# Kernel tuning notes

Hardware: AMD Instinct MI355X
Metric: run time of the kernel (lower is better)

## Reference

```python
import jax, jax.numpy as jnp
import numpy as np

NUM_PROJS = 7
BLOCK = 256       # HyperAttention block_size
SAMPLE = 256      # HyperAttention sample_size
NUM_HEADS = 16

def _hamming_perm(n):
    a = np.array([0, 1])
    for _ in range(n - 1):
        a = np.concatenate([a, a[::-1] + a.max() + 1])
    return a

_PERM = jnp.asarray(_hamming_perm(NUM_PROJS))           # [128] gray-code-ish bucket reorder
_ENC = (2 ** jnp.arange(NUM_PROJS)).astype(jnp.int32)   # [7]

def _lsh_hash(mat, proj_dir):
    # mat: [B,H,N,d], proj_dir: [d,7] -> bucket ids [B,H,N]
    bits = jnp.einsum('bhnd,dr->bhnr', mat, proj_dir) > 0
    ids = (bits * _ENC).sum(-1)
    return _PERM[ids]

def _attn_lse(q, k, v, scale, bias=None):
    s = jnp.einsum('...qd,...kd->...qk', q, k) * scale
    if bias is not None:
        s = s + bias
    lse = jax.nn.logsumexp(s, axis=-1, keepdims=True)
    o = jnp.einsum('...qk,...kd->...qd', jnp.exp(s - lse), v)
    return o, lse

def _gather(t, idx):
    # gather rows along axis 2: out[b,h,s] = t[b,h,idx[b,h,s]]
    return jnp.take_along_axis(t, idx[..., None], axis=2)

def setup_inputs():
    key = jax.random.key(0)
    ks = jax.random.split(key, 7)
    B, L, D, INNER = 2, 8192, 1024, 1024
    x = jax.random.normal(ks[0], (B, L, D), jnp.float32)
    W_qkv = jax.random.normal(ks[1], (D, 3 * INNER), jnp.float32) / np.sqrt(D)
    b_qkv = jnp.zeros((3 * INNER,), jnp.float32)
    W_proj = jax.random.normal(ks[2], (INNER, D), jnp.float32) / np.sqrt(INNER)
    b_proj = jnp.zeros((D,), jnp.float32)
    proj_dir = jax.random.normal(ks[3], (INNER // NUM_HEADS, NUM_PROJS), jnp.float32)
    sampled_set = jax.random.randint(ks[4], (B, NUM_HEADS, SAMPLE), 0, L)
    return {"x": x, "W_qkv": W_qkv, "b_qkv": b_qkv, "W_proj": W_proj,
            "b_proj": b_proj, "proj_dir": proj_dir, "sampled_set": sampled_set}

def reference(x, W_qkv, b_qkv, W_proj, b_proj, proj_dir, sampled_set):
    B, L, D = x.shape
    qkv = (x @ W_qkv + b_qkv).reshape(B, L, 3, NUM_HEADS, -1).transpose(2, 0, 3, 1, 4)
    q, k, v = qkv[0], qkv[1], qkv[2]                      # [B,H,L,dh]
    dh = q.shape[-1]
    scale = dh ** -0.5
    # 1. sortLSH: stable sort q and k rows by angular-LSH bucket id
    q_idx = jnp.argsort(_lsh_hash(q, proj_dir), axis=2, stable=True)
    k_idx = jnp.argsort(_lsh_hash(k, proj_dir), axis=2, stable=True)
    q_idx_inv = jnp.argsort(q_idx, axis=2, stable=True)   # to restore row order
    qs = _gather(q, q_idx)
    ksort = _gather(k, k_idx)
    vsort = _gather(v, k_idx)
    # block-diagonal exact attention over the sorted order (L % BLOCK == 0 here)
    nb = L // BLOCK
    ab, lb = _attn_lse(qs.reshape(B, NUM_HEADS, nb, BLOCK, dh),
                       ksort.reshape(B, NUM_HEADS, nb, BLOCK, dh),
                       vsort.reshape(B, NUM_HEADS, nb, BLOCK, dh), scale)
    attn_block = ab.reshape(B, NUM_HEADS, L, dh)
    lse_block = lb.reshape(B, NUM_HEADS, L, 1)
    # 2. residual uniformly-sampled attention, masking entries already covered by blocks
    k_sub = _gather(ksort, sampled_set)                   # [B,H,SAMPLE,dh]
    v_sub = _gather(vsort, sampled_set)
    blk_q = jnp.arange(L)[None, None, :, None] // BLOCK   # query block id (query_block_size==BLOCK)
    mask = blk_q == (sampled_set // BLOCK)[:, :, None, :]  # [B,H,L,SAMPLE]
    bias = jnp.where(mask, jnp.finfo(x.dtype).min, 0.0).astype(x.dtype)
    attn_res, lse_res = _attn_lse(qs, k_sub, v_sub, scale, bias)
    lse_res = lse_res + jnp.log(jnp.float32(L) / SAMPLE)  # importance weight n_key/sample_size
    # combine the two attentions via their log-sum-exps
    c = 1.0 / (1.0 + jnp.exp(lse_res - lse_block))
    attn = c * attn_block + (1.0 - c) * attn_res
    out = _gather(attn, q_idx_inv)                        # un-sort rows back to input order
    out = out.transpose(0, 2, 1, 3).reshape(B, L, -1)     # [B,L,inner]
    return out @ W_proj + b_proj
```

## Files before the change

kernel.cpp:

```cpp
#include <hip/hip_runtime.h>
#include <hip/hip_fp16.h>
#include <math.h>


typedef _Float16 f16x8 __attribute__((ext_vector_type(8)));
typedef _Float16 f16x4 __attribute__((ext_vector_type(4)));
typedef __fp16 fp16x2 __attribute__((ext_vector_type(2)));
typedef float f32x4 __attribute__((ext_vector_type(4)));

#define WLIST_CAP 524288
#define TAU 0.06f

__device__ __forceinline__ void gl_lds16(const void* g, void* s) {
    __builtin_amdgcn_global_load_lds(
        (const __attribute__((address_space(1))) unsigned int*)g,
        (__attribute__((address_space(3))) unsigned int*)s, 16, 0, 0);
}

__global__ __launch_bounds__(256) void fold_kernel(
    const float* __restrict__ W, const float* __restrict__ bias,
    const float* __restrict__ proj, double* __restrict__ fold,
    double* __restrict__ bfold, _Float16* __restrict__ foldh,
    float* __restrict__ bfold32)
{
    int idx = blockIdx.x * 256 + threadIdx.x;
    if (idx < 2 * 16 * 7 * 1024) {
        int task = idx / 7168;
        int rem = idx - task * 7168;
        int i = rem / 7;
        int r = rem - i * 7;
        int h = task & 15, w = task >> 4;
        double s = 0.0;
        const float* wp = W + (size_t)i * 3072 + w * 1024 + h * 64;
        for (int d = 0; d < 64; ++d)
            s += (double)wp[d] * (double)proj[d * 7 + r];
        fold[idx] = s;
        foldh[((size_t)task * 7 + r) * 1024 + i] = (_Float16)s;
    }
    if (idx < 32768)
        foldh[229376 + idx] = (_Float16)0.f;
    if (idx < 224) {
        int r = idx % 7;
        int task = idx / 7;
        int h = task & 15, w = task >> 4;
        double s = 0.0;
        for (int d = 0; d < 64; ++d)
            s += (double)bias[w * 1024 + h * 64 + d] * (double)proj[d * 7 + r];
        bfold[idx] = s;
        bfold32[idx] = (float)s;
    }
}

__global__ __launch_bounds__(256) void hashext_kernel(
    const float* __restrict__ scores, const float* __restrict__ bfold32,
    int* __restrict__ hq, int* __restrict__ hk,
    int* __restrict__ wcount, int* __restrict__ wlist)
{
    int tid = blockIdx.x * 256 + threadIdx.x;
    int row = tid >> 5, task = tid & 31;
    const float* sp = scores + (size_t)row * 256 + task * 7;
    int id = 0, fl = 0;
#pragma unroll
    for (int r = 0; r < 7; ++r) {
        float val = sp[r] + bfold32[task * 7 + r];
        if (fabsf(val) < TAU) fl = 1;
        if (val > 0.f) id |= (1 << r);
    }
    int hsh = id ^ (id >> 1);
    int w = task >> 4, h = task & 15;
    int b = row >> 13, l = row & 8191;
    (w ? hk : hq)[((size_t)(b * 16 + h) << 13) + l] = hsh;
    if (fl) {
        int slot = atomicAdd(wcount, 1);
        if (slot < WLIST_CAP) wlist[slot] = task * 16384 + row;
    }
}

__global__ __launch_bounds__(256) void refine_kernel(
    const float* __restrict__ x, const double* __restrict__ fold,
    const double* __restrict__ bfold, const int* __restrict__ wcount,
    const int* __restrict__ wlist, int* __restrict__ hq, int* __restrict__ hk)
{
    int n = *wcount;
    if (n > WLIST_CAP) n = WLIST_CAP;
    int lane = threadIdx.x & 63;
    int wid = (blockIdx.x * 256 + threadIdx.x) >> 6;
    int nw = gridDim.x * 4;
    for (int e = wid; e < n; e += nw) {
        int code = wlist[e];
        int task = code >> 14, grow = code & 16383;
        const double* f = fold + (size_t)task * 7168;
        const float* xp = x + (size_t)grow * 1024;
        double acc[7] = {0, 0, 0, 0, 0, 0, 0};
        for (int i = lane; i < 1024; i += 64) {
            double xv = (double)xp[i];
#pragma unroll
            for (int rr = 0; rr < 7; ++rr)
                acc[rr] = fma(xv, f[(size_t)i * 7 + rr], acc[rr]);
        }
        int id = 0;
#pragma unroll
        for (int rr = 0; rr < 7; ++rr) {
            double a = acc[rr];
#pragma unroll
            for (int off = 32; off > 0; off >>= 1) a += __shfl_xor(a, off, 64);
            if (a + bfold[task * 7 + rr] > 0.0) id |= (1 << rr);
        }
        if (lane == 0) {
            int hsh = id ^ (id >> 1);
            int w = task >> 4, h = task & 15;
            int b = grow >> 13, l = grow & 8191;
            (w ? hk : hq)[((size_t)(b * 16 + h) << 13) + l] = hsh;
        }
    }
}

__global__ __launch_bounds__(256) void sort_kernel(
    const int* __restrict__ hq, const int* __restrict__ hk,
    int* __restrict__ qidx, int* __restrict__ kidx,
    int* __restrict__ qrank, int* __restrict__ krank)
{
    __shared__ unsigned short cnt[128][128];
    __shared__ int tot[128];
    __shared__ int base[128];
    int blk = blockIdx.x;
    int sel = blk >> 5, bh = blk & 31;
    const int* hp = (sel ? hk : hq) + ((size_t)bh << 13);
    int* op = (sel ? kidx : qidx) + ((size_t)bh << 13);
    int* rp = (sel ? krank : qrank) + ((size_t)bh << 13);
    int t = threadIdx.x;
    for (int i = t; i < 128 * 128 / 2; i += 256) ((unsigned int*)cnt)[i] = 0u;
    __syncthreads();
    if (t < 128) {
        const int* p = hp + t * 64;
        for (int j = 0; j < 64; ++j) cnt[t][p[j]]++;
    }
    __syncthreads();
    if (t < 128) {
        int run = 0;
        for (int c = 0; c < 128; ++c) {
            int x2 = cnt[c][t];
            cnt[c][t] = (unsigned short)run;
            run += x2;
        }
        tot[t] = run;
    }
    __syncthreads();
    if (t == 0) {
        int run = 0;
        for (int v = 0; v < 128; ++v) { base[v] = run; run += tot[v]; }
    }
    __syncthreads();
    if (t < 128) {
        const int* p = hp + t * 64;
        for (int j = 0; j < 64; ++j) {
            int v = p[j];
            int c = cnt[t][v];
            cnt[t][v] = (unsigned short)(c + 1);
            int pos = base[v] + c;
            op[pos] = t * 64 + j;
            rp[t * 64 + j] = pos;
        }
    }
}

__global__ __launch_bounds__(256) void castx_kernel(
    const float* __restrict__ x, _Float16* __restrict__ xh)
{
    int i = blockIdx.x * 256 + threadIdx.x;
    float4 f = ((const float4*)x)[i];
    _Float16 h4[4] = {(_Float16)f.x, (_Float16)f.y, (_Float16)f.z, (_Float16)f.w};
    *(short4*)&xh[(size_t)i * 4] = *(short4*)h4;
}

__global__ __launch_bounds__(256) void transpose_kernel(
    const float* __restrict__ W, _Float16* __restrict__ Wt, int K, int N)
{
    __shared__ float tile[32][33];
    int bx = blockIdx.x, by = blockIdx.y;
    int tx = threadIdx.x & 31, ty = threadIdx.x >> 5;
    for (int i = ty; i < 32; i += 8)
        tile[i][tx] = W[(size_t)(by * 32 + i) * N + bx * 32 + tx];
    __syncthreads();
    for (int i = ty; i < 32; i += 8)
        Wt[(size_t)(bx * 32 + i) * K + by * 32 + tx] = (_Float16)tile[tx][i];
}

__global__ __launch_bounds__(256) void gather_samp_kernel(
    const _Float16* __restrict__ ks, const _Float16* __restrict__ vs,
    const int* __restrict__ sampled, _Float16* __restrict__ ksamp,
    _Float16* __restrict__ vsamp)
{
    int bh = blockIdx.x;
    int key = blockIdx.y * 64 + (threadIdx.x >> 2);
    int qtr = (threadIdx.x & 3) * 16;
    size_t hb = (size_t)bh << 13;
    int p = sampled[bh * 256 + key];
    size_t src = (hb + p) * 64 + qtr;
    size_t dst = ((size_t)bh * 256 + key) * 64 + qtr;
    *(f16x8*)(ksamp + dst)     = *(const f16x8*)(ks + src);
    *(f16x8*)(ksamp + dst + 8) = *(const f16x8*)(ks + src + 8);
    *(f16x8*)(vsamp + dst)     = *(const f16x8*)(vs + src);
    *(f16x8*)(vsamp + dst + 8) = *(const f16x8*)(vs + src + 8);
}

template <int MODE>
__global__ __launch_bounds__(256) void mfma_gemm(
    const _Float16* __restrict__ A, const _Float16* __restrict__ Bt,
    const float* __restrict__ bias, float* __restrict__ C, int K, int N)
{
    __shared__ __align__(16) _Float16 As[128 * 32];
    __shared__ __align__(16) _Float16 Bs[128 * 32];
    int t = threadIdx.x;
    int w = t >> 6, l = t & 63;
    int m0 = blockIdx.y * 128, n0 = blockIdx.x * 128;
    const _Float16* ga = A + (size_t)(m0 + 32 * w + (l >> 2)) * K + (l & 3) * 8;
    const _Float16* gb = Bt + (size_t)(n0 + 32 * w + (l >> 2)) * K + (l & 3) * 8;
    char* lasA = (char*)As + w * 2048;
    char* lasB = (char*)Bs + w * 2048;
    int wr = w >> 1, wc = w & 1;
    int rl = l & 15, ks = l >> 4;
    f32x4 acc[4][4];
#pragma unroll
    for (int m = 0; m < 4; ++m)
#pragma unroll
        for (int n = 0; n < 4; ++n) acc[m][n] = (f32x4){0.f, 0.f, 0.f, 0.f};
    for (int kk = 0; kk < K; kk += 32) {
        __syncthreads();
        gl_lds16(ga, lasA);
        gl_lds16(ga + 16 * K, lasA + 1024);
        gl_lds16(gb, lasB);
        gl_lds16(gb + 16 * K, lasB + 1024);
        ga += 32; gb += 32;
        __syncthreads();
        f16x8 af[4], bf[4];
#pragma unroll
        for (int m = 0; m < 4; ++m)
            af[m] = *(const f16x8*)((char*)As + (64 * wr + 16 * m + rl) * 64 + ks * 16);
#pragma unroll
        for (int n = 0; n < 4; ++n)
            bf[n] = *(const f16x8*)((char*)Bs + (64 * wc + 16 * n + rl) * 64 + ks * 16);
#pragma unroll
        for (int m = 0; m < 4; ++m)
#pragma unroll
            for (int n = 0; n < 4; ++n)
                acc[m][n] = __builtin_amdgcn_mfma_f32_16x16x32_f16(
                    af[m], bf[n], acc[m][n], 0, 0, 0);
    }
#pragma unroll
    for (int m = 0; m < 4; ++m)
#pragma unroll
        for (int n = 0; n < 4; ++n) {
            int gn = n0 + 64 * wc + 16 * n + rl;
            float bv = (MODE == 2) ? 0.f : bias[gn];
#pragma unroll
            for (int j = 0; j < 4; ++j) {
                int gm = m0 + 64 * wr + 16 * m + 4 * ks + j;
                C[(size_t)gm * N + gn] = acc[m][n][j] + bv;
            }
        }
}

__global__ __launch_bounds__(256) void gemm_qkv_kernel(
    const _Float16* __restrict__ Wt, const _Float16* __restrict__ xh,
    const float* __restrict__ bias, _Float16* __restrict__ Q,
    _Float16* __restrict__ Kb, _Float16* __restrict__ Vb,
    const int* __restrict__ qrank, const int* __restrict__ krank)
{
    const int K = 1024;
    __shared__ __align__(16) _Float16 As[128 * 32];
    __shared__ __align__(16) _Float16 Bs[128 * 32];
    int bid = blockIdx.x;
    int xcd = bid & 7, slot = bid >> 3;
    int y = slot / 3, xl = slot - y * 3;
    int xt = xcd * 3 + xl;
    int m0 = xt * 128;
    int n0 = y * 128;
    int t = threadIdx.x;
    int w = t >> 6, l = t & 63;
    const _Float16* ga = Wt + (size_t)(m0 + 32 * w + (l >> 2)) * K + (l & 3) * 8;
    const _Float16* gb = xh + (size_t)(n0 + 32 * w + (l >> 2)) * K + (l & 3) * 8;
    char* lasA = (char*)As + w * 2048;
    char* lasB = (char*)Bs + w * 2048;
    int wr = w >> 1, wc = w & 1;
    int rl = l & 15, ks = l >> 4;
    int fbase = m0 + 64 * wr;
    int s0 = fbase >> 10;
    int h = (fbase >> 6) & 15;
    int b2 = n0 >> 13;
    const int* rk = (s0 == 0) ? qrank : krank;
    _Float16* dst = (s0 == 0) ? Q : (s0 == 1 ? Kb : Vb);
    size_t bhb = ((size_t)(b2 * 16 + h) << 13);
    int tl = (n0 & 8191) + 64 * wc;
    int pos[4];
#pragma unroll
    for (int n = 0; n < 4; ++n)
        pos[n] = rk[bhb + tl + 16 * n + rl];
    float4 bias4[4];
#pragma unroll
    for (int m = 0; m < 4; ++m)
        bias4[m] = *(const float4*)&bias[fbase + 16 * m + 4 * ks];
    f32x4 acc[4][4];
#pragma unroll
    for (int m = 0; m < 4; ++m)
#pragma unroll
        for (int n = 0; n < 4; ++n) acc[m][n] = (f32x4){0.f, 0.f, 0.f, 0.f};
    for (int kk = 0; kk < K; kk += 32) {
        __syncthreads();
        gl_lds16(ga, lasA);
        gl_lds16(ga + 16 * K, lasA + 1024);
        gl_lds16(gb, lasB);
        gl_lds16(gb + 16 * K, lasB + 1024);
        ga += 32; gb += 32;
        __syncthreads();
        f16x8 af[4], bf[4];
#pragma unroll
        for (int m = 0; m < 4; ++m)
            af[m] = *(const f16x8*)((char*)As + (64 * wr + 16 * m + rl) * 64 + ks * 16);
#pragma unroll
        for (int n = 0; n < 4; ++n)
            bf[n] = *(const f16x8*)((char*)Bs + (64 * wc + 16 * n + rl) * 64 + ks * 16);
#pragma unroll
        for (int m = 0; m < 4; ++m)
#pragma unroll
            for (int n = 0; n < 4; ++n)
                acc[m][n] = __builtin_amdgcn_mfma_f32_16x16x32_f16(
                    af[m], bf[n], acc[m][n], 0, 0, 0);
    }
#pragma unroll
    for (int m = 0; m < 4; ++m)
#pragma unroll
        for (int n = 0; n < 4; ++n) {
            f16x4 st;
            st[0] = (_Float16)(acc[m][n][0] + bias4[m].x);
            st[1] = (_Float16)(acc[m][n][1] + bias4[m].y);
            st[2] = (_Float16)(acc[m][n][2] + bias4[m].z);
            st[3] = (_Float16)(acc[m][n][3] + bias4[m].w);
            *(f16x4*)(dst + (bhb + pos[n]) * 64 + 16 * m + 4 * ks) = st;
        }
}

__global__ __launch_bounds__(256) void attn_mfma_kernel(
    const _Float16* __restrict__ qs_, const _Float16* __restrict__ ks_,
    const _Float16* __restrict__ vs_, const _Float16* __restrict__ ksamp,
    const _Float16* __restrict__ vsamp, const int* __restrict__ qidx,
    const int* __restrict__ sampled, _Float16* __restrict__ pre)
{
    __shared__ __align__(16) _Float16 Vt[2][64 * 68];
    int bid = blockIdx.x;
    int nb = (bid & 7) * 256 + (bid >> 3);
    int bh = nb >> 6, qb = (nb >> 1) & 31, half = nb & 1;
    int bb = bh >> 4, hh = bh & 15;
    size_t hb = (size_t)bh << 13;
    size_t bhs = (size_t)bh * 256;
    int t = threadIdx.x;
    int w = t >> 6, l = t & 63;
    int g = l >> 4, c16 = l & 15;
    int kg = t & 15, dg = t >> 4;
    int qw0 = qb * 256 + half * 128 + w * 32;
    const _Float16 qs = (_Float16)0.125f;

    int orig[2];
    f16x8 qf[2][2];
#pragma unroll
    for (int n = 0; n < 2; ++n) {
        int row = qw0 + 16 * n + c16;
        orig[n] = qidx[hb + row];
        const _Float16* qp = qs_ + (hb + row) * 64 + g * 8;
        qf[n][0] = *(const f16x8*)(qp);
        qf[n][1] = *(const f16x8*)(qp + 32);
#pragma unroll
        for (int j = 0; j < 8; ++j) { qf[n][0][j] *= qs; qf[n][1][j] *= qs; }
    }
    f32x4 o[4][2];
    float mr[2], lr[2];
#pragma unroll
    for (int n = 0; n < 2; ++n) {
        mr[n] = -1e30f; lr[n] = 0.f;
#pragma unroll
        for (int d2 = 0; d2 < 4; ++d2) o[d2][n] = (f32x4){0.f, 0.f, 0.f, 0.f};
    }
    const float LOG32 = 3.4657359027997265f;

    {
        const _Float16* vb = vs_ + (hb + qb * 256) * 64;
        f16x4 vr[4];
#pragma unroll
        for (int j2 = 0; j2 < 4; ++j2)
            vr[j2] = *(const f16x4*)(vb + (4 * kg + j2) * 64 + 4 * dg);
#pragma unroll
        for (int i = 0; i < 4; ++i) {
            f16x4 o4 = {vr[0][i], vr[1][i], vr[2][i], vr[3][i]};
            *(f16x4*)&Vt[0][(4 * dg + i) * 68 + 4 * kg] = o4;
        }
    }

    for (int c = 0; c < 8; ++c) {
        int cur = c & 1, nxt = cur ^ 1;
        bool samp = c >= 4;
        __syncthreads();
        const _Float16* kb = samp ? ksamp + (bhs + (size_t)(c - 4) * 64) * 64
                                  : ks_ + (hb + qb * 256 + (size_t)c * 64) * 64;
        f16x8 kf[4][2];
#pragma unroll
        for (int m = 0; m < 4; ++m) {
            const _Float16* kp = kb + (16 * m + c16) * 64 + g * 8;
            kf[m][0] = *(const f16x8*)(kp);
            kf[m][1] = *(const f16x8*)(kp + 32);
        }
        int4 spv[4];
        if (samp) {
#pragma unroll
            for (int m = 0; m < 4; ++m)
                spv[m] = *(const int4*)(sampled + bhs + (c - 4) * 64 + 16 * m + 4 * g);
        }
        f32x4 sacc[4][2];
#pragma unroll
        for (int m = 0; m < 4; ++m)
#pragma unroll
            for (int n = 0; n < 2; ++n) sacc[m][n] = (f32x4){0.f, 0.f, 0.f, 0.f};
#pragma unroll
        for (int m = 0; m < 4; ++m) {
#pragma unroll
            for (int n = 0; n < 2; ++n)
                sacc[m][n] = __builtin_amdgcn_mfma_f32_16x16x32_f16(
                    kf[m][0], qf[n][0], sacc[m][n], 0, 0, 0);
#pragma unroll
            for (int n = 0; n < 2; ++n)
                sacc[m][n] = __builtin_amdgcn_mfma_f32_16x16x32_f16(
                    kf[m][1], qf[n][1], sacc[m][n], 0, 0, 0);
        }
        f16x4 vrn[4];
        if (c < 7) {
            const _Float16* vb = (c + 1 >= 4)
                ? vsamp + (bhs + (size_t)(c - 3) * 64) * 64
                : vs_ + (hb + qb * 256 + (size_t)(c + 1) * 64) * 64;
#pragma unroll
            for (int j2 = 0; j2 < 4; ++j2)
                vrn[j2] = *(const f16x4*)(vb + (4 * kg + j2) * 64 + 4 * dg);
        }
        f16x4 av[4][4];
#pragma unroll
        for (int m = 0; m < 4; ++m)
#pragma unroll
            for (int d2 = 0; d2 < 4; ++d2)
                av[m][d2] = *(const f16x4*)&Vt[cur][(16 * d2 + c16) * 68 + 16 * m + 4 * g];
        bool msk[4][4];
#pragma unroll
        for (int m = 0; m < 4; ++m) {
            msk[m][0] = samp && ((spv[m].x >> 8) == qb);
            msk[m][1] = samp && ((spv[m].y >> 8) == qb);
            msk[m][2] = samp && ((spv[m].z >> 8) == qb);
            msk[m][3] = samp && ((spv[m].w >> 8) == qb);
        }
        float badd = samp ? LOG32 : 0.f;
#pragma unroll
        for (int n = 0; n < 2; ++n) {
            float sv[16];
#pragma unroll
            for (int m = 0; m < 4; ++m)
#pragma unroll
                for (int r = 0; r < 4; ++r)
                    sv[4 * m + r] = msk[m][r] ? -1e30f : sacc[m][n][r] + badd;
            float a0 = fmaxf(fmaxf(sv[0], sv[1]), sv[2]);
            float a1 = fmaxf(fmaxf(sv[3], sv[4]), sv[5]);
            float a2 = fmaxf(fmaxf(sv[6], sv[7]), sv[8]);
            float a3 = fmaxf(fmaxf(sv[9], sv[10]), sv[11]);
            float a4 = fmaxf(fmaxf(sv[12], sv[13]), sv[14]);
            float cm = fmaxf(fmaxf(fmaxf(a0, a1), a2), fmaxf(fmaxf(a3, a4), sv[15]));
            cm = fmaxf(cm, __shfl_xor(cm, 16, 64));
            cm = fmaxf(cm, __shfl_xor(cm, 32, 64));
            if (__any(cm > mr[n])) {
                float nm = fmaxf(mr[n], cm);
                float fq = __expf(mr[n] - nm);
                mr[n] = nm;
                lr[n] *= fq;
#pragma unroll
                for (int d2 = 0; d2 < 4; ++d2) {
                    o[d2][n][0] *= fq; o[d2][n][1] *= fq;
                    o[d2][n][2] *= fq; o[d2][n][3] *= fq;
                }
            }
            float pv16[16];
#pragma unroll
            for (int r = 0; r < 16; ++r) pv16[r] = __expf(sv[r] - mr[n]);
            float s0 = (pv16[0] + pv16[1]) + (pv16[2] + pv16[3]);
            float s1 = (pv16[4] + pv16[5]) + (pv16[6] + pv16[7]);
            float s2 = (pv16[8] + pv16[9]) + (pv16[10] + pv16[11]);
            float s3 = (pv16[12] + pv16[13]) + (pv16[14] + pv16[15]);
            float ps = (s0 + s1) + (s2 + s3);
            ps += __shfl_xor(ps, 16, 64);
            ps += __shfl_xor(ps, 32, 64);
            lr[n] += ps;
            f16x4 pb[4];
#pragma unroll
            for (int m = 0; m < 4; ++m) {
                fp16x2 c0 = __builtin_amdgcn_cvt_pkrtz(pv16[4 * m + 0], pv16[4 * m + 1]);
                fp16x2 c1 = __builtin_amdgcn_cvt_pkrtz(pv16[4 * m + 2], pv16[4 * m + 3]);
                pb[m][0] = (_Float16)c0[0]; pb[m][1] = (_Float16)c0[1];
                pb[m][2] = (_Float16)c1[0]; pb[m][3] = (_Float16)c1[1];
            }
#pragma unroll
            for (int d2 = 0; d2 < 4; ++d2)
#pragma unroll
                for (int m = 0; m < 4; ++m)
                    o[d2][n] = __builtin_amdgcn_mfma_f32_16x16x16f16(
                        av[m][d2], pb[m], o[d2][n], 0, 0, 0);
        }
        if (c < 7) {
#pragma unroll
            for (int i = 0; i < 4; ++i) {
                f16x4 o4 = {vrn[0][i], vrn[1][i], vrn[2][i], vrn[3][i]};
                *(f16x4*)&Vt[nxt][(4 * dg + i) * 68 + 4 * kg] = o4;
            }
        }
    }
#pragma unroll
    for (int n = 0; n < 2; ++n) {
        float invl = 1.f / lr[n];
        _Float16* pp = pre + ((size_t)(bb * 8192 + orig[n])) * 1024 + hh * 64;
#pragma unroll
        for (int d2 = 0; d2 < 4; ++d2) {
            f16x4 st;
            st[0] = (_Float16)(o[d2][n][0] * invl);
            st[1] = (_Float16)(o[d2][n][1] * invl);
            st[2] = (_Float16)(o[d2][n][2] * invl);
            st[3] = (_Float16)(o[d2][n][3] * invl);
            *(f16x4*)(pp + 16 * d2 + 4 * g) = st;
        }
    }
}

extern "C" void kernel_launch(void* const* d_in, const int* in_sizes, int n_in,
                              void* d_out, int out_size, void* d_ws, size_t ws_size,
                              hipStream_t stream)
{
    (void)in_sizes; (void)n_in; (void)out_size; (void)ws_size;
    const float* x     = (const float*)d_in[0];
    const float* Wqkv  = (const float*)d_in[1];
    const float* bqkv  = (const float*)d_in[2];
    const float* Wproj = (const float*)d_in[3];
    const float* bproj = (const float*)d_in[4];
    const float* proj  = (const float*)d_in[5];
    const int*   samp  = (const int*)d_in[6];
    float* out = (float*)d_out;

    char* ws = (char*)d_ws;
    size_t off = 0;
    auto take = [&](size_t bytes) {
        char* p = ws + off;
        off = (off + bytes + 255) & ~(size_t)255;
        return p;
    };
    _Float16* xh  = (_Float16*)take(33554432);
    _Float16* q   = (_Float16*)take(33554432);
    _Float16* k   = (_Float16*)take(33554432);
    _Float16* v   = (_Float16*)take(33554432);
    float* scores = (float*)take(16777216);
    _Float16* Wtq = (_Float16*)take(6291456);
    _Float16* Wtp = (_Float16*)take(2097152);
    _Float16* foldh = (_Float16*)take(524288);
    _Float16* ksamp = (_Float16*)take(1048576);
    _Float16* vsamp = (_Float16*)take(1048576);
    double* fold   = (double*)take(1835008);
    double* bfold  = (double*)take(1792);
    float* bfold32 = (float*)take(896);
    int* wcount = (int*)take(256);
    int* wlist  = (int*)take(WLIST_CAP * 4);
    int* hq    = (int*)take(1048576);
    int* hk    = (int*)take(1048576);
    int* qidx  = (int*)take(1048576);
    int* kidx  = (int*)take(1048576);
    int* qrank = (int*)take(1048576);
    int* krank = (int*)take(1048576);
    _Float16* pre = xh;

    (void)hipMemsetAsync(wcount, 0, 4, stream);
    castx_kernel<<<dim3(16384), dim3(256), 0, stream>>>(x, xh);
    fold_kernel<<<dim3(896), dim3(256), 0, stream>>>(
        Wqkv, bqkv, proj, fold, bfold, foldh, bfold32);
    mfma_gemm<2><<<dim3(2, 128), dim3(256), 0, stream>>>(
        xh, foldh, nullptr, scores, 1024, 256);
    hashext_kernel<<<dim3(2048), dim3(256), 0, stream>>>(
        scores, bfold32, hq, hk, wcount, wlist);
    refine_kernel<<<dim3(2048), dim3(256), 0, stream>>>(
        x, fold, bfold, wcount, wlist, hq, hk);
    sort_kernel<<<dim3(64), dim3(256), 0, stream>>>(
        hq, hk, qidx, kidx, qrank, krank);
    transpose_kernel<<<dim3(96, 32), dim3(256), 0, stream>>>(Wqkv, Wtq, 1024, 3072);
    transpose_kernel<<<dim3(32, 32), dim3(256), 0, stream>>>(Wproj, Wtp, 1024, 1024);
    gemm_qkv_kernel<<<dim3(3072), dim3(256), 0, stream>>>(
        Wtq, xh, bqkv, q, k, v, qrank, krank);
    gather_samp_kernel<<<dim3(32, 4), dim3(256), 0, stream>>>(
        k, v, samp, ksamp, vsamp);
    attn_mfma_kernel<<<dim3(2048), dim3(256), 0, stream>>>(
        q, k, v, ksamp, vsamp, qidx, samp, pre);
    mfma_gemm<0><<<dim3(8, 128), dim3(256), 0, stream>>>(
        pre, Wtp, bproj, out, 1024, 1024);
}
```

Baseline: 579.0 us.

## Triple-buffer LDS tiles in QKV GEMM to overlap global loads with MFMA

The QKV projection GEMM previously used a single LDS buffer with two barriers per k-step, so each tile load was exposed. It now keeps three LDS stages and prefetches two k-tiles ahead with direct global-to-LDS loads. Each iteration waits on the vmcnt counter and uses a single barrier. This hides memory latency behind the MFMA work, at the cost of three times the LDS footprint, which may lower occupancy, and it relies on manual waitcnt accounting being correct.

```diff
diff --git a/kernel.cpp b/kernel.cpp
--- a/kernel.cpp
+++ b/kernel.cpp
@@ -268,8 +268,8 @@
     const int* __restrict__ qrank, const int* __restrict__ krank)
 {
     const int K = 1024;
-    __shared__ __align__(16) _Float16 As[128 * 32];
-    __shared__ __align__(16) _Float16 Bs[128 * 32];
+    __shared__ __align__(16) _Float16 As[3][128 * 32];
+    __shared__ __align__(16) _Float16 Bs[3][128 * 32];
     int bid = blockIdx.x;
     int xcd = bid & 7, slot = bid >> 3;
     int y = slot / 3, xl = slot - y * 3;
@@ -280,8 +280,7 @@
     int w = t >> 6, l = t & 63;
     const _Float16* ga = Wt + (size_t)(m0 + 32 * w + (l >> 2)) * K + (l & 3) * 8;
     const _Float16* gb = xh + (size_t)(n0 + 32 * w + (l >> 2)) * K + (l & 3) * 8;
-    char* lasA = (char*)As + w * 2048;
-    char* lasB = (char*)Bs + w * 2048;
+    int wOff = w * 2048;
     int wr = w >> 1, wc = w & 1;
     int rl = l & 15, ks = l >> 4;
     int fbase = m0 + 64 * wr;
@@ -305,21 +304,33 @@
     for (int m = 0; m < 4; ++m)
 #pragma unroll
         for (int n = 0; n < 4; ++n) acc[m][n] = (f32x4){0.f, 0.f, 0.f, 0.f};
-    for (int kk = 0; kk < K; kk += 32) {
-        __syncthreads();
-        gl_lds16(ga, lasA);
-        gl_lds16(ga + 16 * K, lasA + 1024);
-        gl_lds16(gb, lasB);
-        gl_lds16(gb + 16 * K, lasB + 1024);
-        ga += 32; gb += 32;
-        __syncthreads();
+
+    auto STAGE = [&](int s, int kk) {
+        gl_lds16(ga + kk, (char*)&As[s][0] + wOff);
+        gl_lds16(ga + kk + 16 * K, (char*)&As[s][0] + wOff + 1024);
+        gl_lds16(gb + kk, (char*)&Bs[s][0] + wOff);
+        gl_lds16(gb + kk + 16 * K, (char*)&Bs[s][0] + wOff + 1024);
+    };
+
+    STAGE(0, 0);
+    STAGE(1, 32);
+    for (int k = 0; k < 32; ++k) {
+        if (k < 31) asm volatile("s_waitcnt vmcnt(4)" ::: "memory");
+        else        asm volatile("s_waitcnt vmcnt(0)" ::: "memory");
+        __builtin_amdgcn_sched_barrier(0);
+        __builtin_amdgcn_s_barrier();
+        __builtin_amdgcn_sched_barrier(0);
+        if (k + 2 < 32) STAGE((k + 2) % 3, (k + 2) * 32);
+        int cur = k % 3;
+        const char* pa = (const char*)&As[cur][0];
+        const char* pb = (const char*)&Bs[cur][0];
         f16x8 af[4], bf[4];
 #pragma unroll
         for (int m = 0; m < 4; ++m)
-            af[m] = *(const f16x8*)((char*)As + (64 * wr + 16 * m + rl) * 64 + ks * 16);
+            af[m] = *(const f16x8*)(pa + (64 * wr + 16 * m + rl) * 64 + ks * 16);
 #pragma unroll
         for (int n = 0; n < 4; ++n)
-            bf[n] = *(const f16x8*)((char*)Bs + (64 * wc + 16 * n + rl) * 64 + ks * 16);
+            bf[n] = *(const f16x8*)(pb + (64 * wc + 16 * n + rl) * 64 + ks * 16);
 #pragma unroll
         for (int m = 0; m < 4; ++m)
 #pragma unroll
```

New measurement: 568.3 us. Within noise of the previous version (-1.9%).
